# Kernel optimization log

Measured on AMD Instinct MI355X. Metric: run time of the kernel, lower is better.

## Reference

```python
import jax, jax.numpy as jnp
import numpy as np

B, N, DIN, DOUT, CHEB_K, EMBED = 64, 2048, 64, 64, 3, 16


def setup_inputs() -> dict:
    key = jax.random.key(0)
    k0, k1, k2, k3 = jax.random.split(key, 4)
    return {
        "x": jax.random.normal(k0, (B, N, DIN), dtype=jnp.float32),
        "node_embeddings": jax.random.normal(k1, (N, EMBED), dtype=jnp.float32),
        "weights_pool": jax.random.normal(k2, (EMBED, CHEB_K, DIN, DOUT), dtype=jnp.float32) * 0.02,
        "bias_pool": jax.random.normal(k3, (EMBED, DOUT), dtype=jnp.float32) * 0.02,
    }


def reference(x, node_embeddings, weights_pool, bias_pool):
    # x: (B, N, dim_in); node_embeddings: (N, embed_dim)
    n = node_embeddings.shape[0]
    # adaptive adjacency: softmax(relu(E E^T)) row-wise
    supports = jax.nn.softmax(jax.nn.relu(node_embeddings @ node_embeddings.T), axis=1)
    # Chebyshev polynomial basis: T0=I, T1=S, Tk = 2 S T_{k-1} - T_{k-2}
    tk = [jnp.eye(n, dtype=x.dtype), supports]
    for _ in range(2, CHEB_K):
        tk.append(2.0 * supports @ tk[-1] - tk[-2])
    S = jnp.stack(tk, axis=0)  # (K, N, N)
    # per-node weights/bias generated from embeddings
    weights = jnp.einsum('nd,dkio->nkio', node_embeddings, weights_pool)  # (N,K,din,dout)
    bias = node_embeddings @ bias_pool  # (N, dout)
    # graph conv: aggregate over neighbors for each Chebyshev order
    x_g = jnp.einsum('knm,bmc->bnkc', S, x)  # (B, N, K, din)
    out = jnp.einsum('bnki,nkio->bno', x_g, weights) + bias  # (B, N, dout)
    return out
```

## Files before the change

kernel.cpp:

```cpp
#include <hip/hip_runtime.h>
#include <hip/hip_bf16.h>

typedef unsigned short u16;
typedef short short8 __attribute__((ext_vector_type(8)));
typedef float floatx4 __attribute__((ext_vector_type(4)));

#define NNODES 2048
#define BATCH  64
#define DIN    64
#define DOUT   64
#define EMB    16

__device__ __forceinline__ u16 f2bf(float f) {
  union { float f; unsigned u; } v; v.f = f;
  unsigned r = v.u + 0x7fffu + ((v.u >> 16) & 1u);
  return (u16)(r >> 16);
}

__device__ __forceinline__ void gload_lds16(const void* g, void* l) {
  __builtin_amdgcn_global_load_lds(
      (const __attribute__((address_space(1))) void*)g,
      (__attribute__((address_space(3))) void*)l, 16, 0, 0);
}

__global__ __launch_bounds__(256) void adj_softmax(const float* __restrict__ E,
                                                   u16* __restrict__ Sb) {
  int n = blockIdx.x, t = threadIdx.x;
  const float4* ep = (const float4*)(E + (size_t)n * EMB);
  float4 e0 = ep[0], e1 = ep[1], e2 = ep[2], e3 = ep[3];

  float lg[8];
  float mx = 0.0f;
#pragma unroll
  for (int j = 0; j < 8; j++) {
    int m = t + j * 256;
    const float4* mp = (const float4*)(E + (size_t)m * EMB);
    float4 a = mp[0], b = mp[1], c = mp[2], d = mp[3];
    float dot = e0.x * a.x + e0.y * a.y + e0.z * a.z + e0.w * a.w
              + e1.x * b.x + e1.y * b.y + e1.z * b.z + e1.w * b.w
              + e2.x * c.x + e2.y * c.y + e2.z * c.z + e2.w * c.w
              + e3.x * d.x + e3.y * d.y + e3.z * d.z + e3.w * d.w;
    dot = fmaxf(dot, 0.0f);
    lg[j] = dot;
    mx = fmaxf(mx, dot);
  }
  __shared__ float smax[4], ssum[4];
#pragma unroll
  for (int off = 32; off > 0; off >>= 1) mx = fmaxf(mx, __shfl_xor(mx, off, 64));
  if ((t & 63) == 0) smax[t >> 6] = mx;
  __syncthreads();
  mx = fmaxf(fmaxf(smax[0], smax[1]), fmaxf(smax[2], smax[3]));

  float sum = 0.0f;
#pragma unroll
  for (int j = 0; j < 8; j++) {
    float e = __expf(lg[j] - mx);
    lg[j] = e;
    sum += e;
  }
#pragma unroll
  for (int off = 32; off > 0; off >>= 1) sum += __shfl_xor(sum, off, 64);
  if ((t & 63) == 0) ssum[t >> 6] = sum;
  __syncthreads();
  sum = ssum[0] + ssum[1] + ssum[2] + ssum[3];
  float inv = 1.0f / sum;
#pragma unroll
  for (int j = 0; j < 8; j++) {
    Sb[(size_t)n * NNODES + t + j * 256] = f2bf(lg[j] * inv);
  }
}

__global__ __launch_bounds__(256) void trans_x(const float* __restrict__ x,
                                               u16* __restrict__ xtt) {
  __shared__ float tile[64][68];
  int b = blockIdx.y;
  int m0 = blockIdx.x * 64;
  int t = threadIdx.x;
  int r = t >> 2, cs = (t & 3) * 16;
  const float* xp = x + ((size_t)b * NNODES + m0 + r) * DIN + cs;
  float4 v0 = ((const float4*)xp)[0];
  float4 v1 = ((const float4*)xp)[1];
  float4 v2 = ((const float4*)xp)[2];
  float4 v3 = ((const float4*)xp)[3];
  *(float4*)&tile[r][cs]      = v0;
  *(float4*)&tile[r][cs + 4]  = v1;
  *(float4*)&tile[r][cs + 8]  = v2;
  *(float4*)&tile[r][cs + 12] = v3;
  __syncthreads();
  int c = t >> 2, ms = (t & 3) * 16;
  short8 o0, o1;
#pragma unroll
  for (int j = 0; j < 8; j++) o0[j] = (short)f2bf(tile[ms + j][c]);
#pragma unroll
  for (int j = 0; j < 8; j++) o1[j] = (short)f2bf(tile[ms + 8 + j][c]);
  u16* op = xtt + ((size_t)b * 64 + c) * NNODES + m0 + ms;
  *(short8*)op = o0;
  *(short8*)(op + 8) = o1;
}

__global__ __launch_bounds__(256) void trans_bf(const u16* __restrict__ in,
                                                u16* __restrict__ out,
                                                int R, int C) {
  __shared__ u16 tile[64][72];
  int r0 = blockIdx.y * 64, c0 = blockIdx.x * 64;
  int t = threadIdx.x;
  int r = t >> 2, cs = (t & 3) * 16;
  const u16* ip = in + (size_t)(r0 + r) * C + c0 + cs;
  *(short8*)&tile[r][cs]     = *(const short8*)ip;
  *(short8*)&tile[r][cs + 8] = *(const short8*)(ip + 8);
  __syncthreads();
  int c = t >> 2, ms = (t & 3) * 16;
  short8 o0, o1;
#pragma unroll
  for (int j = 0; j < 8; j++) o0[j] = (short)tile[ms + j][c];
#pragma unroll
  for (int j = 0; j < 8; j++) o1[j] = (short)tile[ms + 8 + j][c];
  u16* op = out + (size_t)(c0 + c) * R + r0 + ms;
  *(short8*)op = o0;
  *(short8*)(op + 8) = o1;
}

__global__ __launch_bounds__(256) void peff_k(const float* __restrict__ pool,
                                              float* __restrict__ peff) {
  int idx = blockIdx.x * 256 + threadIdx.x;
  int d = idx / 12288;
  int r = idx - d * 12288;
  int o = r / 192;
  int ki = r - o * 192;
  int k = ki >> 6, i = ki & 63;
  float p = pool[(size_t)d * 12288 + k * 4096 + i * 64 + o];
  if (k == 0) p -= pool[(size_t)d * 12288 + 8192 + i * 64 + o];
  if (k == 2) p += p;
  peff[idx] = p;
}

__global__ __launch_bounds__(256) void wgen2(const float* __restrict__ E,
                                             const float* __restrict__ peff,
                                             u16* __restrict__ W) {
  __shared__ float Es[128][17];
  int t = threadIdx.x;
  int n0 = blockIdx.y * 128;
  for (int idx = t; idx < 128 * EMB; idx += 256)
    Es[idx >> 4][idx & 15] = E[(size_t)n0 * EMB + idx];
  int e = blockIdx.x * 256 + t;
  float pv[16];
#pragma unroll
  for (int d = 0; d < 16; d++) pv[d] = peff[(size_t)d * 12288 + e];
  __syncthreads();
#pragma unroll 4
  for (int nn = 0; nn < 128; nn++) {
    float acc = 0.0f;
#pragma unroll
    for (int d = 0; d < 16; d++) acc = fmaf(Es[nn][d], pv[d], acc);
    W[(size_t)(n0 + nn) * 12288 + e] = f2bf(acc);
  }
}

#define GK 2048
#define GN 4096
#define NT 32
#define BUFU 24576

__global__ __launch_bounds__(512) void gemm_dp(const u16* __restrict__ A,
                                               const u16* __restrict__ Bt,
                                               u16* __restrict__ C) {
  __shared__ u16 smem[3 * BUFU];
  int t = threadIdx.x, lane = t & 63, wave = t >> 6;

  int lin = blockIdx.y * gridDim.x + blockIdx.x;
  int nwg = gridDim.x * gridDim.y;
  int sw = (lin & 7) * (nwg >> 3) + (lin >> 3);
  int bx = sw & 31, by = sw >> 5;
  int m0 = by * 256, n0 = bx * 128;

  const u16* pg[6];
  int lof[6];
#pragma unroll
  for (int j = 0; j < 4; j++) {
    int c = t + 512 * j;
    int row = c >> 3;
    int gs = (c & 7) ^ (row & 7);
    pg[j] = A + (size_t)(m0 + row) * GK + gs * 8;
    lof[j] = c * 8;
  }
#pragma unroll
  for (int j = 0; j < 2; j++) {
    int c = t + 512 * j;
    int row = c >> 3;
    int gs = (c & 7) ^ (row & 7);
    pg[4 + j] = Bt + (size_t)(n0 + row) * GK + gs * 8;
    lof[4 + j] = 16384 + c * 8;
  }

  auto stage = [&](int b, int kt) {
#pragma unroll
    for (int j = 0; j < 6; j++)
      gload_lds16(pg[j] + kt, &smem[b * BUFU + lof[j]]);
  };

  int wr = wave >> 1, wc = wave & 1;
  int lr = lane & 15, lg = lane >> 4;

  floatx4 acc[4][4];
#pragma unroll
  for (int mi = 0; mi < 4; mi++)
#pragma unroll
    for (int ni = 0; ni < 4; ni++) acc[mi][ni] = (floatx4)0.0f;

  int aoff[2][4], boff[2][4];
#pragma unroll
  for (int s = 0; s < 2; s++) {
#pragma unroll
    for (int mi = 0; mi < 4; mi++) {
      int row = wr * 64 + mi * 16 + lr;
      int slot = s * 4 + lg;
      aoff[s][mi] = row * 64 + (slot ^ (row & 7)) * 8;
    }
#pragma unroll
    for (int ni = 0; ni < 4; ni++) {
      int row = wc * 64 + ni * 16 + lr;
      int slot = s * 4 + lg;
      boff[s][ni] = 16384 + row * 64 + (slot ^ (row & 7)) * 8;
    }
  }

  auto compute = [&](int b) {
    const u16* base = &smem[b * BUFU];
    short8 af[2][4], bf[2][4];
#pragma unroll
    for (int s = 0; s < 2; s++) {
#pragma unroll
      for (int mi = 0; mi < 4; mi++) af[s][mi] = *(const short8*)(base + aoff[s][mi]);
#pragma unroll
      for (int ni = 0; ni < 4; ni++) bf[s][ni] = *(const short8*)(base + boff[s][ni]);
    }
#pragma unroll
    for (int s = 0; s < 2; s++)
#pragma unroll
      for (int mi = 0; mi < 4; mi++)
#pragma unroll
        for (int ni = 0; ni < 4; ni++)
          acc[mi][ni] = __builtin_amdgcn_mfma_f32_16x16x32_bf16(af[s][mi], bf[s][ni],
                                                                acc[mi][ni], 0, 0, 0);
  };

  stage(0, 0);
  stage(1, 64);

  for (int tt = 0; tt < NT - 2; ++tt) {
    asm volatile("s_waitcnt vmcnt(6)" ::: "memory");
    __builtin_amdgcn_s_barrier();
    stage((tt + 2) % 3, (tt + 2) * 64);
    compute(tt % 3);
  }
  asm volatile("s_waitcnt vmcnt(6)" ::: "memory");
  __builtin_amdgcn_s_barrier();
  compute((NT - 2) % 3);
  asm volatile("s_waitcnt vmcnt(0)" ::: "memory");
  __builtin_amdgcn_s_barrier();
  compute((NT - 1) % 3);

#pragma unroll
  for (int mi = 0; mi < 4; mi++)
#pragma unroll
    for (int ni = 0; ni < 4; ni++) {
      int row = m0 + wr * 64 + mi * 16 + lg * 4;
      int col = n0 + wc * 64 + ni * 16 + lr;
#pragma unroll
      for (int r = 0; r < 4; r++)
        C[(size_t)(row + r) * GN + col] = f2bf(acc[mi][ni][r]);
    }
}

__global__ __launch_bounds__(256) void final_k(const float* __restrict__ x,
                                               const float* __restrict__ E,
                                               const float* __restrict__ bpool,
                                               const u16* __restrict__ xg1,
                                               const u16* __restrict__ xg2,
                                               const u16* __restrict__ W,
                                               float* __restrict__ out) {
  __shared__ u16 Xs[3][64][72];
  __shared__ u16 Ws[64][200];
  __shared__ float bias_s[64];
  int n = blockIdx.x, t = threadIdx.x;

  {
    int b = t >> 2, i0 = (t & 3) * 16;
    const float* xp = x + ((size_t)b * NNODES + n) * DIN + i0;
    float4 v0 = ((const float4*)xp)[0];
    float4 v1 = ((const float4*)xp)[1];
    float4 v2 = ((const float4*)xp)[2];
    float4 v3 = ((const float4*)xp)[3];
    u16* d = &Xs[0][b][i0];
    d[0] = f2bf(v0.x); d[1] = f2bf(v0.y); d[2] = f2bf(v0.z); d[3] = f2bf(v0.w);
    d[4] = f2bf(v1.x); d[5] = f2bf(v1.y); d[6] = f2bf(v1.z); d[7] = f2bf(v1.w);
    d[8] = f2bf(v2.x); d[9] = f2bf(v2.y); d[10] = f2bf(v2.z); d[11] = f2bf(v2.w);
    d[12] = f2bf(v3.x); d[13] = f2bf(v3.y); d[14] = f2bf(v3.z); d[15] = f2bf(v3.w);
  }
  for (int idx = t; idx < 512; idx += 256) {
    short8 v1 = *(const short8*)(xg1 + (size_t)n * 4096 + idx * 8);
    *(short8*)&Xs[1][idx >> 3][(idx & 7) * 8] = v1;
    short8 v2 = *(const short8*)(xg2 + (size_t)n * 4096 + idx * 8);
    *(short8*)&Xs[2][idx >> 3][(idx & 7) * 8] = v2;
  }
  for (int idx = t; idx < 1536; idx += 256) {
    short8 v = *(const short8*)(W + (size_t)n * 12288 + idx * 8);
    int o = idx / 24, w8 = idx - o * 24;
    *(short8*)&Ws[o][w8 * 8] = v;
  }
  if (t < 64) {
    float acc = 0.0f;
#pragma unroll
    for (int d = 0; d < 16; d++)
      acc = fmaf(E[(size_t)n * EMB + d], bpool[d * 64 + t], acc);
    bias_s[t] = acc;
  }
  __syncthreads();

  int lane = t & 63, wave = t >> 6;
  int lr = lane & 15, lg = lane >> 4;
  int wb = wave * 16;
  floatx4 acc[4];
#pragma unroll
  for (int ot = 0; ot < 4; ot++) acc[ot] = (floatx4)0.0f;

#pragma unroll
  for (int ks = 0; ks < 6; ks++) {
    int kk = ks * 32 + lg * 8;
    short8 a = *(const short8*)&Xs[kk >> 6][wb + lr][kk & 63];
#pragma unroll
    for (int ot = 0; ot < 4; ot++) {
      short8 bb = *(const short8*)&Ws[ot * 16 + lr][kk];
      acc[ot] = __builtin_amdgcn_mfma_f32_16x16x32_bf16(a, bb, acc[ot], 0, 0, 0);
    }
  }
#pragma unroll
  for (int ot = 0; ot < 4; ot++) {
    int o = ot * 16 + lr;
    float bs = bias_s[o];
#pragma unroll
    for (int r = 0; r < 4; r++) {
      int b = wb + lg * 4 + r;
      out[((size_t)b * NNODES + n) * DOUT + o] = acc[ot][r] + bs;
    }
  }
}

extern "C" void kernel_launch(void* const* d_in, const int* in_sizes, int n_in,
                              void* d_out, int out_size, void* d_ws, size_t ws_size,
                              hipStream_t stream) {
  const float* x     = (const float*)d_in[0];
  const float* E     = (const float*)d_in[1];
  const float* pool  = (const float*)d_in[2];
  const float* bpool = (const float*)d_in[3];
  float* out = (float*)d_out;

  char* ws = (char*)d_ws;
  u16* Sb   = (u16*)(ws);
  u16* xtt  = (u16*)(ws + 8388608);
  u16* xg1  = (u16*)(ws + 25165824);
  u16* xg1t = (u16*)(ws + 41943040);
  u16* xg2  = (u16*)(ws + 58720256);
  u16* Wall = (u16*)(ws + 75497472);
  float* peff = (float*)(ws + 58720256);

  peff_k<<<768, 256, 0, stream>>>(pool, peff);
  adj_softmax<<<NNODES, 256, 0, stream>>>(E, Sb);
  trans_x<<<dim3(NNODES / 64, BATCH), 256, 0, stream>>>(x, xtt);
  wgen2<<<dim3(48, NNODES / 128), 256, 0, stream>>>(E, peff, Wall);
  gemm_dp<<<dim3(32, 8), 512, 0, stream>>>(Sb, xtt, xg1);
  trans_bf<<<dim3(4096 / 64, NNODES / 64), 256, 0, stream>>>(xg1, xg1t, NNODES, 4096);
  gemm_dp<<<dim3(32, 8), 512, 0, stream>>>(Sb, xg1t, xg2);
  final_k<<<NNODES, 256, 0, stream>>>(x, E, bpool, xg1, xg2, Wall, out);
}
```

Before: 173.7 us.

## Fuse xg1 transpose into GEMM epilogue and split main loop into interleaved phases

The separate bf16 transpose kernel is removed. The first GEMM now also writes a transposed copy of its output tile through a per-wave LDS scratch buffer, which saves one launch and a full read and write of the 16 MB intermediate. The GEMM main loop is also split into two half-K phases, with the global-to-LDS prefetch spread across them, extra barriers between them, and s_setprio raised around the MFMA blocks to improve overlap. The price is a heavier epilogue in the first GEMM and one more barrier per k-step.

```diff
diff --git a/kernel.cpp b/kernel.cpp
--- a/kernel.cpp
+++ b/kernel.cpp
@@ -98,28 +98,6 @@
   *(short8*)(op + 8) = o1;
 }
 
-__global__ __launch_bounds__(256) void trans_bf(const u16* __restrict__ in,
-                                                u16* __restrict__ out,
-                                                int R, int C) {
-  __shared__ u16 tile[64][72];
-  int r0 = blockIdx.y * 64, c0 = blockIdx.x * 64;
-  int t = threadIdx.x;
-  int r = t >> 2, cs = (t & 3) * 16;
-  const u16* ip = in + (size_t)(r0 + r) * C + c0 + cs;
-  *(short8*)&tile[r][cs]     = *(const short8*)ip;
-  *(short8*)&tile[r][cs + 8] = *(const short8*)(ip + 8);
-  __syncthreads();
-  int c = t >> 2, ms = (t & 3) * 16;
-  short8 o0, o1;
-#pragma unroll
-  for (int j = 0; j < 8; j++) o0[j] = (short)tile[ms + j][c];
-#pragma unroll
-  for (int j = 0; j < 8; j++) o1[j] = (short)tile[ms + 8 + j][c];
-  u16* op = out + (size_t)(c0 + c) * R + r0 + ms;
-  *(short8*)op = o0;
-  *(short8*)(op + 8) = o1;
-}
-
 __global__ __launch_bounds__(256) void peff_k(const float* __restrict__ pool,
                                               float* __restrict__ peff) {
   int idx = blockIdx.x * 256 + threadIdx.x;
@@ -163,7 +141,8 @@
 
 __global__ __launch_bounds__(512) void gemm_dp(const u16* __restrict__ A,
                                                const u16* __restrict__ Bt,
-                                               u16* __restrict__ C) {
+                                               u16* __restrict__ C,
+                                               u16* __restrict__ Ct) {
   __shared__ u16 smem[3 * BUFU];
   int t = threadIdx.x, lane = t & 63, wave = t >> 6;
 
@@ -192,12 +171,6 @@
     lof[4 + j] = 16384 + c * 8;
   }
 
-  auto stage = [&](int b, int kt) {
-#pragma unroll
-    for (int j = 0; j < 6; j++)
-      gload_lds16(pg[j] + kt, &smem[b * BUFU + lof[j]]);
-  };
-
   int wr = wave >> 1, wc = wave & 1;
   int lr = lane & 15, lg = lane >> 4;
 
@@ -224,41 +197,51 @@
     }
   }
 
-  auto compute = [&](int b) {
-    const u16* base = &smem[b * BUFU];
-    short8 af[2][4], bf[2][4];
-#pragma unroll
-    for (int s = 0; s < 2; s++) {
-#pragma unroll
-      for (int mi = 0; mi < 4; mi++) af[s][mi] = *(const short8*)(base + aoff[s][mi]);
-#pragma unroll
-      for (int ni = 0; ni < 4; ni++) bf[s][ni] = *(const short8*)(base + boff[s][ni]);
-    }
-#pragma unroll
-    for (int s = 0; s < 2; s++)
-#pragma unroll
-      for (int mi = 0; mi < 4; mi++)
-#pragma unroll
-        for (int ni = 0; ni < 4; ni++)
-          acc[mi][ni] = __builtin_amdgcn_mfma_f32_16x16x32_bf16(af[s][mi], bf[s][ni],
-                                                                acc[mi][ni], 0, 0, 0);
+  auto phase = [&](int bufc, int s, int bufs, int kt, int jlo, bool do_stage) {
+    const u16* base = &smem[bufc * BUFU];
+    short8 af[4], bf[4];
+#pragma unroll
+    for (int mi = 0; mi < 4; mi++) af[mi] = *(const short8*)(base + aoff[s][mi]);
+#pragma unroll
+    for (int ni = 0; ni < 4; ni++) bf[ni] = *(const short8*)(base + boff[s][ni]);
+    if (do_stage) {
+#pragma unroll
+      for (int j = 0; j < 3; j++)
+        gload_lds16(pg[jlo + j] + kt, &smem[bufs * BUFU + lof[jlo + j]]);
+    }
+    __builtin_amdgcn_s_setprio(1);
+#pragma unroll
+    for (int mi = 0; mi < 4; mi++)
+#pragma unroll
+      for (int ni = 0; ni < 4; ni++)
+        acc[mi][ni] = __builtin_amdgcn_mfma_f32_16x16x32_bf16(af[mi], bf[ni],
+                                                              acc[mi][ni], 0, 0, 0);
+    __builtin_amdgcn_s_setprio(0);
   };
 
-  stage(0, 0);
-  stage(1, 64);
+#pragma unroll
+  for (int j = 0; j < 6; j++) gload_lds16(pg[j], &smem[lof[j]]);
+#pragma unroll
+  for (int j = 0; j < 6; j++) gload_lds16(pg[j] + 64, &smem[BUFU + lof[j]]);
 
   for (int tt = 0; tt < NT - 2; ++tt) {
+    int bufc = tt % 3, bufs = (tt + 2) % 3;
     asm volatile("s_waitcnt vmcnt(6)" ::: "memory");
     __builtin_amdgcn_s_barrier();
-    stage((tt + 2) % 3, (tt + 2) * 64);
-    compute(tt % 3);
+    phase(bufc, 0, bufs, (tt + 2) * 64, 0, true);
+    __builtin_amdgcn_s_barrier();
+    phase(bufc, 1, bufs, (tt + 2) * 64, 3, true);
   }
   asm volatile("s_waitcnt vmcnt(6)" ::: "memory");
   __builtin_amdgcn_s_barrier();
-  compute((NT - 2) % 3);
+  phase((NT - 2) % 3, 0, 0, 0, 0, false);
+  __builtin_amdgcn_s_barrier();
+  phase((NT - 2) % 3, 1, 0, 0, 0, false);
   asm volatile("s_waitcnt vmcnt(0)" ::: "memory");
   __builtin_amdgcn_s_barrier();
-  compute((NT - 1) % 3);
+  phase((NT - 1) % 3, 0, 0, 0, 0, false);
+  __builtin_amdgcn_s_barrier();
+  phase((NT - 1) % 3, 1, 0, 0, 0, false);
 
 #pragma unroll
   for (int mi = 0; mi < 4; mi++)
@@ -270,6 +253,27 @@
       for (int r = 0; r < 4; r++)
         C[(size_t)(row + r) * GN + col] = f2bf(acc[mi][ni][r]);
     }
+
+  if (Ct) {
+    __syncthreads();
+    u16* scr = smem + wave * 64 * 72;
+#pragma unroll
+    for (int mi = 0; mi < 4; mi++)
+#pragma unroll
+      for (int ni = 0; ni < 4; ni++) {
+        int ncol = ni * 16 + lr;
+#pragma unroll
+        for (int r = 0; r < 4; r++)
+          scr[ncol * 72 + mi * 16 + lg * 4 + r] = f2bf(acc[mi][ni][r]);
+      }
+    int c = lane;
+    u16* op = Ct + (size_t)(n0 + wc * 64 + c) * GK + m0 + wr * 64;
+#pragma unroll
+    for (int jj = 0; jj < 8; jj++) {
+      short8 v = *(const short8*)&scr[c * 72 + jj * 8];
+      *(short8*)(op + jj * 8) = v;
+    }
+  }
 }
 
 __global__ __launch_bounds__(256) void final_k(const float* __restrict__ x,
@@ -368,8 +372,7 @@
   adj_softmax<<<NNODES, 256, 0, stream>>>(E, Sb);
   trans_x<<<dim3(NNODES / 64, BATCH), 256, 0, stream>>>(x, xtt);
   wgen2<<<dim3(48, NNODES / 128), 256, 0, stream>>>(E, peff, Wall);
-  gemm_dp<<<dim3(32, 8), 512, 0, stream>>>(Sb, xtt, xg1);
-  trans_bf<<<dim3(4096 / 64, NNODES / 64), 256, 0, stream>>>(xg1, xg1t, NNODES, 4096);
-  gemm_dp<<<dim3(32, 8), 512, 0, stream>>>(Sb, xg1t, xg2);
+  gemm_dp<<<dim3(32, 8), 512, 0, stream>>>(Sb, xtt, xg1, xg1t);
+  gemm_dp<<<dim3(32, 8), 512, 0, stream>>>(Sb, xg1t, xg2, nullptr);
   final_k<<<NNODES, 256, 0, stream>>>(x, E, bpool, xg1, xg2, Wall, out);
 }
```

Result: no change. 170.5 us (-1.8%).

## Merge prologue kernels and fuse xg1 transpose into GEMM epilogue

Applied to the files above, without the earlier changes.

Folds the adjacency softmax, x transpose and pool-permute kernels into one launch, with the work chosen by block index. The standalone transpose of the first GEMM's output is removed. Instead the GEMM epilogue stages its accumulator tile through LDS with an XOR swizzle and writes a transposed copy directly. This cuts two launches and a full read/write pass over the 16 MB intermediate, at the cost of extra LDS traffic and a barrier in the first GEMM's epilogue.

```diff
diff --git a/kernel.cpp b/kernel.cpp
--- a/kernel.cpp
+++ b/kernel.cpp
@@ -3,6 +3,7 @@
 
 typedef unsigned short u16;
 typedef short short8 __attribute__((ext_vector_type(8)));
+typedef short short4v __attribute__((ext_vector_type(4)));
 typedef float floatx4 __attribute__((ext_vector_type(4)));
 
 #define NNODES 2048
@@ -23,115 +24,95 @@
       (__attribute__((address_space(3))) void*)l, 16, 0, 0);
 }
 
-__global__ __launch_bounds__(256) void adj_softmax(const float* __restrict__ E,
-                                                   u16* __restrict__ Sb) {
-  int n = blockIdx.x, t = threadIdx.x;
-  const float4* ep = (const float4*)(E + (size_t)n * EMB);
-  float4 e0 = ep[0], e1 = ep[1], e2 = ep[2], e3 = ep[3];
-
-  float lg[8];
-  float mx = 0.0f;
-#pragma unroll
-  for (int j = 0; j < 8; j++) {
-    int m = t + j * 256;
-    const float4* mp = (const float4*)(E + (size_t)m * EMB);
-    float4 a = mp[0], b = mp[1], c = mp[2], d = mp[3];
-    float dot = e0.x * a.x + e0.y * a.y + e0.z * a.z + e0.w * a.w
-              + e1.x * b.x + e1.y * b.y + e1.z * b.z + e1.w * b.w
-              + e2.x * c.x + e2.y * c.y + e2.z * c.z + e2.w * c.w
-              + e3.x * d.x + e3.y * d.y + e3.z * d.z + e3.w * d.w;
-    dot = fmaxf(dot, 0.0f);
-    lg[j] = dot;
-    mx = fmaxf(mx, dot);
-  }
-  __shared__ float smax[4], ssum[4];
-#pragma unroll
-  for (int off = 32; off > 0; off >>= 1) mx = fmaxf(mx, __shfl_xor(mx, off, 64));
-  if ((t & 63) == 0) smax[t >> 6] = mx;
-  __syncthreads();
-  mx = fmaxf(fmaxf(smax[0], smax[1]), fmaxf(smax[2], smax[3]));
-
-  float sum = 0.0f;
-#pragma unroll
-  for (int j = 0; j < 8; j++) {
-    float e = __expf(lg[j] - mx);
-    lg[j] = e;
-    sum += e;
-  }
-#pragma unroll
-  for (int off = 32; off > 0; off >>= 1) sum += __shfl_xor(sum, off, 64);
-  if ((t & 63) == 0) ssum[t >> 6] = sum;
-  __syncthreads();
-  sum = ssum[0] + ssum[1] + ssum[2] + ssum[3];
-  float inv = 1.0f / sum;
-#pragma unroll
-  for (int j = 0; j < 8; j++) {
-    Sb[(size_t)n * NNODES + t + j * 256] = f2bf(lg[j] * inv);
-  }
-}
-
-__global__ __launch_bounds__(256) void trans_x(const float* __restrict__ x,
-                                               u16* __restrict__ xtt) {
-  __shared__ float tile[64][68];
-  int b = blockIdx.y;
-  int m0 = blockIdx.x * 64;
+__global__ __launch_bounds__(256) void prologue(const float* __restrict__ E,
+                                                const float* __restrict__ pool,
+                                                const float* __restrict__ x,
+                                                u16* __restrict__ Sb,
+                                                u16* __restrict__ xtt,
+                                                float* __restrict__ peff) {
+  int bid = blockIdx.x;
   int t = threadIdx.x;
-  int r = t >> 2, cs = (t & 3) * 16;
-  const float* xp = x + ((size_t)b * NNODES + m0 + r) * DIN + cs;
-  float4 v0 = ((const float4*)xp)[0];
-  float4 v1 = ((const float4*)xp)[1];
-  float4 v2 = ((const float4*)xp)[2];
-  float4 v3 = ((const float4*)xp)[3];
-  *(float4*)&tile[r][cs]      = v0;
-  *(float4*)&tile[r][cs + 4]  = v1;
-  *(float4*)&tile[r][cs + 8]  = v2;
-  *(float4*)&tile[r][cs + 12] = v3;
-  __syncthreads();
-  int c = t >> 2, ms = (t & 3) * 16;
-  short8 o0, o1;
-#pragma unroll
-  for (int j = 0; j < 8; j++) o0[j] = (short)f2bf(tile[ms + j][c]);
-#pragma unroll
-  for (int j = 0; j < 8; j++) o1[j] = (short)f2bf(tile[ms + 8 + j][c]);
-  u16* op = xtt + ((size_t)b * 64 + c) * NNODES + m0 + ms;
-  *(short8*)op = o0;
-  *(short8*)(op + 8) = o1;
-}
-
-__global__ __launch_bounds__(256) void trans_bf(const u16* __restrict__ in,
-                                                u16* __restrict__ out,
-                                                int R, int C) {
-  __shared__ u16 tile[64][72];
-  int r0 = blockIdx.y * 64, c0 = blockIdx.x * 64;
-  int t = threadIdx.x;
-  int r = t >> 2, cs = (t & 3) * 16;
-  const u16* ip = in + (size_t)(r0 + r) * C + c0 + cs;
-  *(short8*)&tile[r][cs]     = *(const short8*)ip;
-  *(short8*)&tile[r][cs + 8] = *(const short8*)(ip + 8);
-  __syncthreads();
-  int c = t >> 2, ms = (t & 3) * 16;
-  short8 o0, o1;
-#pragma unroll
-  for (int j = 0; j < 8; j++) o0[j] = (short)tile[ms + j][c];
-#pragma unroll
-  for (int j = 0; j < 8; j++) o1[j] = (short)tile[ms + 8 + j][c];
-  u16* op = out + (size_t)(c0 + c) * R + r0 + ms;
-  *(short8*)op = o0;
-  *(short8*)(op + 8) = o1;
-}
-
-__global__ __launch_bounds__(256) void peff_k(const float* __restrict__ pool,
-                                              float* __restrict__ peff) {
-  int idx = blockIdx.x * 256 + threadIdx.x;
-  int d = idx / 12288;
-  int r = idx - d * 12288;
-  int o = r / 192;
-  int ki = r - o * 192;
-  int k = ki >> 6, i = ki & 63;
-  float p = pool[(size_t)d * 12288 + k * 4096 + i * 64 + o];
-  if (k == 0) p -= pool[(size_t)d * 12288 + 8192 + i * 64 + o];
-  if (k == 2) p += p;
-  peff[idx] = p;
+
+  if (bid < 2048) {
+    int n = bid;
+    const float4* ep = (const float4*)(E + (size_t)n * EMB);
+    float4 e0 = ep[0], e1 = ep[1], e2 = ep[2], e3 = ep[3];
+    float lg[8];
+    float mx = 0.0f;
+#pragma unroll
+    for (int j = 0; j < 8; j++) {
+      int m = t + j * 256;
+      const float4* mp = (const float4*)(E + (size_t)m * EMB);
+      float4 a = mp[0], b = mp[1], c = mp[2], d = mp[3];
+      float dot = e0.x * a.x + e0.y * a.y + e0.z * a.z + e0.w * a.w
+                + e1.x * b.x + e1.y * b.y + e1.z * b.z + e1.w * b.w
+                + e2.x * c.x + e2.y * c.y + e2.z * c.z + e2.w * c.w
+                + e3.x * d.x + e3.y * d.y + e3.z * d.z + e3.w * d.w;
+      dot = fmaxf(dot, 0.0f);
+      lg[j] = dot;
+      mx = fmaxf(mx, dot);
+    }
+    __shared__ float smax[4], ssum[4];
+#pragma unroll
+    for (int off = 32; off > 0; off >>= 1) mx = fmaxf(mx, __shfl_xor(mx, off, 64));
+    if ((t & 63) == 0) smax[t >> 6] = mx;
+    __syncthreads();
+    mx = fmaxf(fmaxf(smax[0], smax[1]), fmaxf(smax[2], smax[3]));
+    float sum = 0.0f;
+#pragma unroll
+    for (int j = 0; j < 8; j++) {
+      float e = __expf(lg[j] - mx);
+      lg[j] = e;
+      sum += e;
+    }
+#pragma unroll
+    for (int off = 32; off > 0; off >>= 1) sum += __shfl_xor(sum, off, 64);
+    if ((t & 63) == 0) ssum[t >> 6] = sum;
+    __syncthreads();
+    sum = ssum[0] + ssum[1] + ssum[2] + ssum[3];
+    float inv = 1.0f / sum;
+#pragma unroll
+    for (int j = 0; j < 8; j++)
+      Sb[(size_t)n * NNODES + t + j * 256] = f2bf(lg[j] * inv);
+
+  } else if (bid < 4096) {
+    __shared__ float tile[64][68];
+    int u = bid - 2048;
+    int b = u >> 5;
+    int m0 = (u & 31) * 64;
+    int r = t >> 2, cs = (t & 3) * 16;
+    const float* xp = x + ((size_t)b * NNODES + m0 + r) * DIN + cs;
+    float4 v0 = ((const float4*)xp)[0];
+    float4 v1 = ((const float4*)xp)[1];
+    float4 v2 = ((const float4*)xp)[2];
+    float4 v3 = ((const float4*)xp)[3];
+    *(float4*)&tile[r][cs]      = v0;
+    *(float4*)&tile[r][cs + 4]  = v1;
+    *(float4*)&tile[r][cs + 8]  = v2;
+    *(float4*)&tile[r][cs + 12] = v3;
+    __syncthreads();
+    int c = t >> 2, ms = (t & 3) * 16;
+    short8 o0, o1;
+#pragma unroll
+    for (int j = 0; j < 8; j++) o0[j] = (short)f2bf(tile[ms + j][c]);
+#pragma unroll
+    for (int j = 0; j < 8; j++) o1[j] = (short)f2bf(tile[ms + 8 + j][c]);
+    u16* op = xtt + ((size_t)b * 64 + c) * NNODES + m0 + ms;
+    *(short8*)op = o0;
+    *(short8*)(op + 8) = o1;
+
+  } else {
+    int idx = (bid - 4096) * 256 + t;
+    int d = idx / 12288;
+    int r = idx - d * 12288;
+    int o = r / 192;
+    int ki = r - o * 192;
+    int k = ki >> 6, i = ki & 63;
+    float p = pool[(size_t)d * 12288 + k * 4096 + i * 64 + o];
+    if (k == 0) p -= pool[(size_t)d * 12288 + 8192 + i * 64 + o];
+    if (k == 2) p += p;
+    peff[idx] = p;
+  }
 }
 
 __global__ __launch_bounds__(256) void wgen2(const float* __restrict__ E,
@@ -163,7 +144,8 @@
 
 __global__ __launch_bounds__(512) void gemm_dp(const u16* __restrict__ A,
                                                const u16* __restrict__ Bt,
-                                               u16* __restrict__ C) {
+                                               u16* __restrict__ C,
+                                               u16* __restrict__ Ct) {
   __shared__ u16 smem[3 * BUFU];
   int t = threadIdx.x, lane = t & 63, wave = t >> 6;
 
@@ -270,6 +252,30 @@
       for (int r = 0; r < 4; r++)
         C[(size_t)(row + r) * GN + col] = f2bf(acc[mi][ni][r]);
     }
+
+  if (Ct) {
+    __syncthreads();
+    u16* scr = smem + wave * 4096;
+#pragma unroll
+    for (int mi = 0; mi < 4; mi++)
+#pragma unroll
+      for (int ni = 0; ni < 4; ni++) {
+        int ncol = ni * 16 + lr;
+        int chunk = mi * 2 + (lg >> 1);
+        int off = ncol * 64 + ((chunk ^ (ncol & 7)) << 3) + (lg & 1) * 4;
+        short4v sv;
+#pragma unroll
+        for (int r = 0; r < 4; r++) sv[r] = (short)f2bf(acc[mi][ni][r]);
+        *(short4v*)&scr[off] = sv;
+      }
+    int c = lane;
+    u16* op = Ct + (size_t)(n0 + wc * 64 + c) * GK + m0 + wr * 64;
+#pragma unroll
+    for (int jj = 0; jj < 8; jj++) {
+      short8 v = *(const short8*)&scr[c * 64 + ((jj ^ (c & 7)) << 3)];
+      *(short8*)(op + jj * 8) = v;
+    }
+  }
 }
 
 __global__ __launch_bounds__(256) void final_k(const float* __restrict__ x,
@@ -364,12 +370,9 @@
   u16* Wall = (u16*)(ws + 75497472);
   float* peff = (float*)(ws + 58720256);
 
-  peff_k<<<768, 256, 0, stream>>>(pool, peff);
-  adj_softmax<<<NNODES, 256, 0, stream>>>(E, Sb);
-  trans_x<<<dim3(NNODES / 64, BATCH), 256, 0, stream>>>(x, xtt);
+  prologue<<<4864, 256, 0, stream>>>(E, pool, x, Sb, xtt, peff);
   wgen2<<<dim3(48, NNODES / 128), 256, 0, stream>>>(E, peff, Wall);
-  gemm_dp<<<dim3(32, 8), 512, 0, stream>>>(Sb, xtt, xg1);
-  trans_bf<<<dim3(4096 / 64, NNODES / 64), 256, 0, stream>>>(xg1, xg1t, NNODES, 4096);
-  gemm_dp<<<dim3(32, 8), 512, 0, stream>>>(Sb, xg1t, xg2);
+  gemm_dp<<<dim3(32, 8), 512, 0, stream>>>(Sb, xtt, xg1, xg1t);
+  gemm_dp<<<dim3(32, 8), 512, 0, stream>>>(Sb, xg1t, xg2, nullptr);
   final_k<<<NNODES, 256, 0, stream>>>(x, E, bpool, xg1, xg2, Wall, out);
 }
```

After: 163.7 us. 5.8% less time.
